# Kernel tuning notes

Hardware: AMD Instinct MI355X
Metric: run time of the kernel (lower is better)

## Reference

```python
import jax, jax.numpy as jnp
import numpy as np

B = 4
G = 1024                      # GridSize
H = 1.0 / (G - 1)             # h = (right-left)/(GridSize-1), area=[[0,0],[1,1]]
GD = 0.0                      # boundary value for hard_encode padding


def _cross(a):
    # sum of 4-neighborhood: matches conv2d with kernel [[0,.5,0],[.5,0,.5],[0,.5,0]] / 0.5
    return a[..., :-2, 1:-1] + a[..., 2:, 1:-1] + a[..., 1:-1, :-2] + a[..., 1:-1, 2:]


def _inner(a):
    return a[..., 1:-1, 1:-1]


def kappa(x, mu):
    # assumed parameterization (kappa undefined in source): exp(mu * x)
    return jnp.exp(mu * x)


def setup_inputs() -> dict:
    key = jax.random.key(0)
    k1, k2, k3, k4 = jax.random.split(key, 4)
    pre = jax.random.normal(k1, (B, 1, G - 2, G - 2), jnp.float32)
    f = jax.random.normal(k2, (B, 1, G, G), jnp.float32)
    mu = jax.random.uniform(k3, (1,), jnp.float32)
    prev_pre = jax.random.normal(k4, (B, 1, G, G), jnp.float32) * 0.1
    return {"pre": pre, "f": f, "mu": mu, "prev_pre": prev_pre, "maxiter": 20}


def reference(pre, f, mu, prev_pre, maxiter):
    # w = kappa(prev_pre, mu) is iteration-invariant -> hoist out of the loop
    w = kappa(prev_pre, mu)            # [B,1,G,G]
    w_in = _inner(w)                   # [B,1,G-2,G-2]
    force = _inner(f) * (H * H)
    # k3 conv: 0.5*cross + 2*center
    y3 = 0.5 * _cross(w) + 2.0 * w_in

    def step(y, _):
        u = jnp.pad(y, ((0, 0), (0, 0), (1, 1), (1, 1)), constant_values=GD)
        y1 = 0.5 * _cross(u) * w_in    # conv(u, k1) * w_inner
        y2 = 0.5 * _cross(w * u)       # conv(w*u, k2)
        return (force + y1 + y2) / y3, None

    # original: one jac_step, then `maxiter` more -> maxiter+1 total
    y, _ = jax.lax.scan(step, pre, None, length=maxiter + 1)
    return y
```

## Files before the change

### kernel.cpp

```cpp
#include <hip/hip_runtime.h>

#define BB 4
#define GG 1024
#define NI 1022
#define SROW 1024
#define HH2 (2.0f / (1023.0f * 1023.0f))
#define OFF 12
#define TBR 64
#define TBC 128
#define TOUTR 40
#define TOUTC 104
#define NTR 26
#define NTC 10
#define HS 132

typedef float vf4 __attribute__((ext_vector_type(4)));
typedef float vf2 __attribute__((ext_vector_type(2)));

__device__ __forceinline__ float dpp_left(float x) {
    int i = __builtin_bit_cast(int, x);
    i = __builtin_amdgcn_update_dpp(i, i, 0x138, 0xf, 0xf, false);
    return __builtin_bit_cast(float, i);
}
__device__ __forceinline__ float dpp_right(float x) {
    int i = __builtin_bit_cast(int, x);
    i = __builtin_amdgcn_update_dpp(i, i, 0x130, 0xf, 0xf, false);
    return __builtin_bit_cast(float, i);
}

template<int TKP, bool VIN4, bool VOUT4>
__global__ __launch_bounds__(512, 4)
void pinn_slab(const float* __restrict__ ysrc,
               const float* __restrict__ fglob,
               const float* __restrict__ mu_p,
               const float* __restrict__ pp,
               float* __restrict__ yout)
{
    __shared__ float wh0[16 * HS], wh1[16 * HS];
    __shared__ float ytop[2][16 * HS], ybot[2][16 * HS];

    const int tid = threadIdx.x;
    const int tx = tid & 31, ty = tid >> 5;
    const int b  = blockIdx.z;
    const int AR = blockIdx.y * TOUTR - OFF;
    const int A0 = blockIdx.x * TOUTC - OFF;
    const int R  = 4 * ty;
    const int c0 = 4 * tx;
    const float mu = mu_p[0];

    const int cb = min(max(A0 + c0, 0), GG - 4);
    const size_t pb = (size_t)b * GG * GG;
    const int r0 = min(max(AR + R,     0), GG - 1);
    const int r1 = min(max(AR + R + 1, 0), GG - 1);
    const int r2 = min(max(AR + R + 2, 0), GG - 1);
    const int r3 = min(max(AR + R + 3, 0), GG - 1);
    const int r4 = min(max(AR + R + 4, 0), GG - 1);
    vf4 wv0 = *(const vf4*)&pp[pb + (size_t)r0 * GG + cb];
    vf4 wv1 = *(const vf4*)&pp[pb + (size_t)r1 * GG + cb];
    vf4 wv2 = *(const vf4*)&pp[pb + (size_t)r2 * GG + cb];
    vf4 wv3 = *(const vf4*)&pp[pb + (size_t)r3 * GG + cb];
    const vf4 fv0 = *(const vf4*)&fglob[pb + (size_t)r1 * GG + cb];
    const vf4 fv1 = *(const vf4*)&fglob[pb + (size_t)r2 * GG + cb];
    const vf4 fv2 = *(const vf4*)&fglob[pb + (size_t)r3 * GG + cb];
    const vf4 fv3 = *(const vf4*)&fglob[pb + (size_t)r4 * GG + cb];

    vf4 y0v, y1v, y2v, y3v;
    {
        const int i0 = min(max(AR + R,     0), NI - 1);
        const int i1 = min(max(AR + R + 1, 0), NI - 1);
        const int i2 = min(max(AR + R + 2, 0), NI - 1);
        const int i3 = min(max(AR + R + 3, 0), NI - 1);
        if (VIN4) {
            const int cy = min(max(A0 + c0, 0), SROW - 4);
            y0v = *(const vf4*)&ysrc[(size_t)(b * NI + i0) * SROW + cy];
            y1v = *(const vf4*)&ysrc[(size_t)(b * NI + i1) * SROW + cy];
            y2v = *(const vf4*)&ysrc[(size_t)(b * NI + i2) * SROW + cy];
            y3v = *(const vf4*)&ysrc[(size_t)(b * NI + i3) * SROW + cy];
        } else {
            const int cy  = min(max(A0 + c0, 0), NI - 2);
            const int cy2 = min(cy + 2, NI - 2);
            #define LDY(dst, ii) { \
                const size_t base_ = (size_t)(b * NI + (ii)) * NI; \
                const vf2 a_ = *(const vf2*)&ysrc[base_ + cy]; \
                const vf2 b_ = *(const vf2*)&ysrc[base_ + cy2]; \
                dst[0] = a_[0]; dst[1] = a_[1]; dst[2] = b_[0]; dst[3] = b_[1]; }
            LDY(y0v, i0) LDY(y1v, i1) LDY(y2v, i2) LDY(y3v, i3)
            #undef LDY
        }
    }

    #pragma unroll
    for (int m = 0; m < 4; ++m) {
        wv0[m] = __expf(mu * wv0[m]);
        wv1[m] = __expf(mu * wv1[m]);
        wv2[m] = __expf(mu * wv2[m]);
        wv3[m] = __expf(mu * wv3[m]);
    }
    *(vf4*)&wh0[ty * HS + c0] = wv0;
    *(vf4*)&wh1[ty * HS + c0] = wv1;
    __syncthreads();

    const int nxt = min(ty + 1, 15) * HS + c0;
    const vf4 w4 = *(const vf4*)&wh0[nxt];
    const vf4 w5 = *(const vf4*)&wh1[nxt];

    const float s1_0 = dpp_right(wv0[0]);
    const float s1_1 = dpp_right(wv1[0]);
    const float s1_2 = dpp_right(wv2[0]);
    const float s1_3 = dpp_right(wv3[0]);
    const float s1_4 = dpp_right(w4[0]);
    const float s1_5 = dpp_right(w5[0]);
    const float s2_1 = dpp_right(wv1[1]);
    const float s2_2 = dpp_right(wv2[1]);
    const float s2_3 = dpp_right(wv3[1]);
    const float s2_4 = dpp_right(w4[1]);
    const float sf0 = dpp_right(fv0[0]);
    const float sf1 = dpp_right(fv1[0]);
    const float sf2 = dpp_right(fv2[0]);
    const float sf3 = dpp_right(fv3[0]);

    vf4 bN0,bN1,bN2,bN3, bS0,bS1,bS2,bS3, bW0,bW1,bW2,bW3,
        bE0,bE1,bE2,bE3, bf0,bf1,bf2,bf3;

    #define COEFF(kk, N_, C_, S_, s1N, s1C, s1S, s2C, FV, SF, BN, BS, BW, BE, BF, YV) { \
        const vf4 wN = {N_[1], N_[2], N_[3], s1N}; \
        const vf4 wW = C_; \
        const vf4 wC = {C_[1], C_[2], C_[3], s1C}; \
        const vf4 wE = {C_[2], C_[3], s1C, s2C}; \
        const vf4 wS = {S_[1], S_[2], S_[3], s1S}; \
        const vf4 aN = wC + wN, aS = wC + wS, aW = wC + wW, aE = wC + wE; \
        const vf4 den = (aN + aS) + (aW + aE); \
        const int gi = AR + R + (kk); \
        vf4 rd; \
        _Pragma("unroll") \
        for (int m = 0; m < 4; ++m) { \
            float x = __builtin_amdgcn_rcpf(den[m]); \
            x = x * (2.0f - den[m] * x); \
            const int gj = A0 + c0 + m; \
            const bool in = (gi >= 0) && (gi < NI) && (gj >= 0) && (gj < NI); \
            rd[m] = in ? x : 0.0f; \
            YV[m] = in ? YV[m] : 0.0f; \
        } \
        BN = aN * rd; BS = aS * rd; BW = aW * rd; BE = aE * rd; \
        const vf4 fC = {FV[1], FV[2], FV[3], SF}; \
        BF = (fC * rd) * HH2; }

    COEFF(0, wv0, wv1, wv2, s1_0, s1_1, s1_2, s2_1, fv0, sf0, bN0,bS0,bW0,bE0,bf0, y0v)
    COEFF(1, wv1, wv2, wv3, s1_1, s1_2, s1_3, s2_2, fv1, sf1, bN1,bS1,bW1,bE1,bf1, y1v)
    COEFF(2, wv2, wv3, w4,  s1_2, s1_3, s1_4, s2_3, fv2, sf2, bN2,bS2,bW2,bE2,bf2, y2v)
    COEFF(3, wv3, w4,  w5,  s1_3, s1_4, s1_5, s2_4, fv3, sf3, bN3,bS3,bW3,bE3,bf3, y3v)
    #undef COEFF

    const int tyo = ty * HS + c0;
    const int upo = max(ty - 1, 0)  * HS + c0;
    const int dno = min(ty + 1, 15) * HS + c0;

    for (int t = 1; t <= TKP; ++t) {
        float* tb = ytop[t & 1];
        float* bb = ybot[t & 1];
        *(vf4*)&tb[tyo] = y0v;
        *(vf4*)&bb[tyo] = y3v;
        __syncthreads();
        const vf4 up = *(const vf4*)&bb[upo];
        const vf4 dn = *(const vf4*)&tb[dno];
        const vf4 yW0 = {dpp_left(y0v[3]), y0v[0], y0v[1], y0v[2]};
        const vf4 yW1 = {dpp_left(y1v[3]), y1v[0], y1v[1], y1v[2]};
        const vf4 yW2 = {dpp_left(y2v[3]), y2v[0], y2v[1], y2v[2]};
        const vf4 yW3 = {dpp_left(y3v[3]), y3v[0], y3v[1], y3v[2]};
        const vf4 yE0 = {y0v[1], y0v[2], y0v[3], dpp_right(y0v[0])};
        const vf4 yE1 = {y1v[1], y1v[2], y1v[3], dpp_right(y1v[0])};
        const vf4 yE2 = {y2v[1], y2v[2], y2v[3], dpp_right(y2v[0])};
        const vf4 yE3 = {y3v[1], y3v[2], y3v[3], dpp_right(y3v[0])};
        vf4 n0 = bf0; n0 += bN0 * up;  n0 += bS0 * y1v; n0 += bW0 * yW0; n0 += bE0 * yE0;
        vf4 n1 = bf1; n1 += bN1 * y0v; n1 += bS1 * y2v; n1 += bW1 * yW1; n1 += bE1 * yE1;
        vf4 n2 = bf2; n2 += bN2 * y1v; n2 += bS2 * y3v; n2 += bW2 * yW2; n2 += bE2 * yE2;
        vf4 n3 = bf3; n3 += bN3 * y2v; n3 += bS3 * dn;  n3 += bW3 * yW3; n3 += bE3 * yE3;
        y0v = n0; y1v = n1; y2v = n2; y3v = n3;
    }

    if (R >= OFF && R < OFF + TOUTR && c0 >= OFF && c0 < OFF + TOUTC) {
        const int gj0 = A0 + c0;
        if (VOUT4) {
            #define STORE4(kk, YV) { \
                const int gi = AR + R + (kk); \
                if (gi < NI && gj0 <= SROW - 4) \
                    *(vf4*)&yout[(size_t)(b * NI + gi) * SROW + gj0] = YV; }
            STORE4(0, y0v) STORE4(1, y1v) STORE4(2, y2v) STORE4(3, y3v)
            #undef STORE4
        } else {
            #define STORE(kk, YV) { \
                const int gi = AR + R + (kk); \
                if (gi < NI) { \
                    const size_t rb = (size_t)(b * NI + gi) * NI; \
                    if (gj0 + 3 < NI) { \
                        vf2 pa, pv; pa[0]=YV[0]; pa[1]=YV[1]; pv[0]=YV[2]; pv[1]=YV[3]; \
                        *(vf2*)&yout[rb + gj0] = pa; *(vf2*)&yout[rb + gj0 + 2] = pv; \
                    } else { \
                        _Pragma("unroll") \
                        for (int m = 0; m < 4; ++m) \
                            if (gj0 + m < NI) yout[rb + gj0 + m] = YV[m]; \
                    } \
                } }
            STORE(0, y0v) STORE(1, y1v) STORE(2, y2v) STORE(3, y3v)
            #undef STORE
        }
    }
}

extern "C" void kernel_launch(void* const* d_in, const int* in_sizes, int n_in,
                              void* d_out, int out_size, void* d_ws, size_t ws_size,
                              hipStream_t stream) {
    const float* pre = (const float*)d_in[0];
    const float* f   = (const float*)d_in[1];
    const float* mu  = (const float*)d_in[2];
    const float* pp  = (const float*)d_in[3];

    float* yA = (float*)d_ws;

    const dim3 grid(NTC, NTR, BB);
    const dim3 bs(512, 1, 1);
    pinn_slab<11, false, true ><<<grid, bs, 0, stream>>>(pre, f, mu, pp, yA);
    pinn_slab<10, true,  false><<<grid, bs, 0, stream>>>(yA,  f, mu, pp, (float*)d_out);
}
```

Before: 155.0 us.

## Size row halo per pass to iteration count and alias weight smem buffers

The row halo offset and output tile height become template parameters, set to match the number of temporally fused iterations in each pass (11/42 and 10/44). This produces more valid output rows per block and fewer row tiles (25 and 24 instead of 26), cutting redundant halo recomputation. The weight shared-memory arrays are now aliased onto the y halo buffers, which lowers LDS use per block but depends on their lifetimes not overlapping. The store guards now check the row window per row instead of per 4-row group.

After: 147.1 us. 5.1% less time.

```diff
diff --git a/kernel.cpp b/kernel.cpp
--- a/kernel.cpp
+++ b/kernel.cpp
@@ -5,12 +5,10 @@
 #define NI 1022
 #define SROW 1024
 #define HH2 (2.0f / (1023.0f * 1023.0f))
-#define OFF 12
+#define OFFC 12
 #define TBR 64
 #define TBC 128
-#define TOUTR 40
 #define TOUTC 104
-#define NTR 26
 #define NTC 10
 #define HS 132
 
@@ -28,7 +26,7 @@
     return __builtin_bit_cast(float, i);
 }
 
-template<int TKP, bool VIN4, bool VOUT4>
+template<int TKP, int OFFR, int TOUTR, bool VIN4, bool VOUT4>
 __global__ __launch_bounds__(512, 4)
 void pinn_slab(const float* __restrict__ ysrc,
                const float* __restrict__ fglob,
@@ -36,14 +34,15 @@
                const float* __restrict__ pp,
                float* __restrict__ yout)
 {
-    __shared__ float wh0[16 * HS], wh1[16 * HS];
     __shared__ float ytop[2][16 * HS], ybot[2][16 * HS];
+    float* const wh0 = ytop[0];
+    float* const wh1 = ybot[0];
 
     const int tid = threadIdx.x;
     const int tx = tid & 31, ty = tid >> 5;
     const int b  = blockIdx.z;
-    const int AR = blockIdx.y * TOUTR - OFF;
-    const int A0 = blockIdx.x * TOUTC - OFF;
+    const int AR = blockIdx.y * TOUTR - OFFR;
+    const int A0 = blockIdx.x * TOUTC - OFFC;
     const int R  = 4 * ty;
     const int c0 = 4 * tx;
     const float mu = mu_p[0];
@@ -178,29 +177,33 @@
         y0v = n0; y1v = n1; y2v = n2; y3v = n3;
     }
 
-    if (R >= OFF && R < OFF + TOUTR && c0 >= OFF && c0 < OFF + TOUTC) {
+    if (c0 >= OFFC && c0 < OFFC + TOUTC) {
         const int gj0 = A0 + c0;
         if (VOUT4) {
             #define STORE4(kk, YV) { \
-                const int gi = AR + R + (kk); \
-                if (gi < NI && gj0 <= SROW - 4) \
-                    *(vf4*)&yout[(size_t)(b * NI + gi) * SROW + gj0] = YV; }
+                const int r = R + (kk); \
+                if (r >= OFFR && r < OFFR + TOUTR) { \
+                    const int gi = AR + r; \
+                    if (gi < NI && gj0 <= SROW - 4) \
+                        *(vf4*)&yout[(size_t)(b * NI + gi) * SROW + gj0] = YV; } }
             STORE4(0, y0v) STORE4(1, y1v) STORE4(2, y2v) STORE4(3, y3v)
             #undef STORE4
         } else {
             #define STORE(kk, YV) { \
-                const int gi = AR + R + (kk); \
-                if (gi < NI) { \
-                    const size_t rb = (size_t)(b * NI + gi) * NI; \
-                    if (gj0 + 3 < NI) { \
-                        vf2 pa, pv; pa[0]=YV[0]; pa[1]=YV[1]; pv[0]=YV[2]; pv[1]=YV[3]; \
-                        *(vf2*)&yout[rb + gj0] = pa; *(vf2*)&yout[rb + gj0 + 2] = pv; \
-                    } else { \
-                        _Pragma("unroll") \
-                        for (int m = 0; m < 4; ++m) \
-                            if (gj0 + m < NI) yout[rb + gj0 + m] = YV[m]; \
-                    } \
-                } }
+                const int r = R + (kk); \
+                if (r >= OFFR && r < OFFR + TOUTR) { \
+                    const int gi = AR + r; \
+                    if (gi < NI) { \
+                        const size_t rb = (size_t)(b * NI + gi) * NI; \
+                        if (gj0 + 3 < NI) { \
+                            vf2 pa, pv; pa[0]=YV[0]; pa[1]=YV[1]; pv[0]=YV[2]; pv[1]=YV[3]; \
+                            *(vf2*)&yout[rb + gj0] = pa; *(vf2*)&yout[rb + gj0 + 2] = pv; \
+                        } else { \
+                            _Pragma("unroll") \
+                            for (int m = 0; m < 4; ++m) \
+                                if (gj0 + m < NI) yout[rb + gj0 + m] = YV[m]; \
+                        } \
+                    } } }
             STORE(0, y0v) STORE(1, y1v) STORE(2, y2v) STORE(3, y3v)
             #undef STORE
         }
@@ -217,8 +220,7 @@
 
     float* yA = (float*)d_ws;
 
-    const dim3 grid(NTC, NTR, BB);
     const dim3 bs(512, 1, 1);
-    pinn_slab<11, false, true ><<<grid, bs, 0, stream>>>(pre, f, mu, pp, yA);
-    pinn_slab<10, true,  false><<<grid, bs, 0, stream>>>(yA,  f, mu, pp, (float*)d_out);
-}
+    pinn_slab<11, 11, 42, false, true ><<<dim3(NTC, 25, BB), bs, 0, stream>>>(pre, f, mu, pp, yA);
+    pinn_slab<10, 10, 44, true,  false><<<dim3(NTC, 24, BB), bs, 0, stream>>>(yA,  f, mu, pp, (float*)d_out);
+}
```
